# Kernel optimization log

Measured on AMD Instinct MI355X. Metric: run time of the kernel, lower is better.

Reference implementation:

```python
import jax, jax.numpy as jnp
import numpy as np


def setup_inputs() -> dict:
    key = jax.random.key(0)
    k1, k2 = jax.random.split(key)
    X_query = jax.random.normal(k1, (4, 4096, 32), dtype=jnp.float32)
    X_fit = jax.random.normal(k2, (4, 4096, 32), dtype=jnp.float32)
    return {"X_query": X_query, "X_fit": X_fit}


def _bandwidth(X_fit):
    # Silverman-style rule as in the torch module (bandwith init arg == 0.0)
    b, n, d = X_fit.shape
    flat = X_fit.reshape(b, -1)
    # torch.quantile with no dim reduces over the whole tensor -> scalar
    q = jnp.quantile(flat, 0.75) - jnp.quantile(flat, 0.25)
    std = jnp.std(X_fit, axis=(1, 2), ddof=1)  # torch.std is unbiased -> [b]
    return 0.9 * jnp.minimum(std, q / 1.34) / (n ** 0.2)  # [b]


def reference(X_query, X_fit):
    # fit()
    bw = _bandwidth(X_fit)                       # [b]
    nmu2 = jnp.sum(X_fit * X_fit, axis=-1)       # [b, m]
    # score()
    nx2 = jnp.sum(X_query * X_query, axis=-1, keepdims=True)   # [b, n, 1]
    dot = jnp.einsum('bnd,bmd->bnm', X_query, X_fit)           # [b, n, m]
    dist = nx2 + nmu2[:, None, :] - 2.0 * dot                  # [b, n, m]
    return jnp.sum(jnp.exp(-dist / bw[:, None, None]), axis=-1)  # [b, n]
```

## Files before the change

### kernel.cpp

```cpp
#include <hip/hip_runtime.h>
#include <hip/hip_bf16.h>
#include <math.h>

#define BB 4
#define MM 4096
#define DD 32
#define NSLOT 64

#define LOA -0.6945f
#define HIA -0.6545f
#define LOB  0.6545f
#define HIB  0.6945f

#define PSUM_OFF    0
#define PSUMSQ_OFF  1024
#define PBELA_OFF   2048
#define PBELB_OFF   3072
#define PCNTA_OFF   4096
#define PCNTB_OFF   5120
#define COEF_OFF    6144
#define CANDA_OFF   8192
#define CANDB_OFF   (CANDA_OFF + 65536)
#define NMU2_OFF    (CANDB_OFF + 65536)
#define NX2_OFF     (NMU2_OFF + 65536)
#define QH_OFF      (NX2_OFF + 65536)
#define QL_OFF      (QH_OFF + 1048576)
#define FH_OFF      (QL_OFF + 1048576)
#define FL_OFF      (FH_OFF + 1048576)

typedef short bf16x8 __attribute__((ext_vector_type(8)));
typedef float f32x4  __attribute__((ext_vector_type(4)));

__device__ __forceinline__ void cvt8(float4 a, float4 b, bf16x8* hi, bf16x8* lo) {
    union U { bf16x8 v; __hip_bfloat162 p[4]; };
    U H, L;
    float2 xs[4] = {make_float2(a.x,a.y), make_float2(a.z,a.w),
                    make_float2(b.x,b.y), make_float2(b.z,b.w)};
    #pragma unroll
    for (int i = 0; i < 4; i++) {
        __hip_bfloat162 h = __float22bfloat162_rn(xs[i]);
        float2 hf = __bfloat1622float2(h);
        H.p[i] = h;
        L.p[i] = __float22bfloat162_rn(make_float2(xs[i].x - hf.x, xs[i].y - hf.y));
    }
    *hi = H.v; *lo = L.v;
}

__global__ __launch_bounds__(256) void k_prep(
    const float* __restrict__ Xq, const float* __restrict__ Xf,
    short* __restrict__ Qh, short* __restrict__ Ql,
    short* __restrict__ Fh, short* __restrict__ Fl,
    float* __restrict__ nmu2, float* __restrict__ nx2,
    float* __restrict__ psum, float* __restrict__ psumsq,
    unsigned int* __restrict__ pbelA, unsigned int* __restrict__ pbelB,
    unsigned int* __restrict__ pcntA, unsigned int* __restrict__ pcntB,
    float* __restrict__ candA, float* __restrict__ candB)
{
    int tid = threadIdx.x;

    if (blockIdx.x >= 256) {
        int t = (blockIdx.x - 256) * 256 + tid;
        const float4* src = (const float4*)Xq + (size_t)t * 2;
        float4 v0 = src[0], v1 = src[1];
        bf16x8 hi, lo; cvt8(v0, v1, &hi, &lo);
        ((bf16x8*)Qh)[t] = hi;
        ((bf16x8*)Ql)[t] = lo;
        float xs[8] = {v0.x, v0.y, v0.z, v0.w, v1.x, v1.y, v1.z, v1.w};
        float s2 = 0.f;
        #pragma unroll
        for (int c = 0; c < 8; c++) s2 = fmaf(xs[c], xs[c], s2);
        s2 += __shfl_xor(s2, 1);
        s2 += __shfl_xor(s2, 2);
        if ((t & 3) == 0) nx2[t >> 2] = s2;
        return;
    }

    __shared__ float rs[256], rs2[256];
    __shared__ float lA[NSLOT], lB[NSLOT];
    __shared__ unsigned int lcA, lcB, lbA, lbB;
    if (tid == 0) { lcA = 0; lcB = 0; lbA = 0; lbB = 0; }
    __syncthreads();

    int blk = blockIdx.x;
    int t = blk * 256 + tid;
    const float4* src = (const float4*)Xf + (size_t)t * 2;
    float4 v0 = src[0], v1 = src[1];
    bf16x8 hi, lo; cvt8(v0, v1, &hi, &lo);
    ((bf16x8*)Fh)[t] = hi;
    ((bf16x8*)Fl)[t] = lo;

    float xs[8] = {v0.x, v0.y, v0.z, v0.w, v1.x, v1.y, v1.z, v1.w};
    float s = 0.f, s2 = 0.f;
    unsigned int belA = 0, belB = 0;
    #pragma unroll
    for (int c = 0; c < 8; c++) {
        float x = xs[c];
        s += x;
        s2 = fmaf(x, x, s2);
        belA += (x < LOA) ? 1u : 0u;
        belB += (x < LOB) ? 1u : 0u;
        if (x >= LOA && x < HIA) { unsigned int p = atomicAdd(&lcA, 1u); if (p < NSLOT) lA[p] = x; }
        if (x >= LOB && x < HIB) { unsigned int p = atomicAdd(&lcB, 1u); if (p < NSLOT) lB[p] = x; }
    }
    float r = s2;
    r += __shfl_xor(r, 1);
    r += __shfl_xor(r, 2);
    if ((t & 3) == 0) nmu2[t >> 2] = r;

    unsigned int wa = belA, wb = belB;
    #pragma unroll
    for (int m = 1; m < 64; m <<= 1) { wa += __shfl_xor(wa, m); wb += __shfl_xor(wb, m); }
    if ((tid & 63) == 0) { atomicAdd(&lbA, wa); atomicAdd(&lbB, wb); }

    rs[tid] = s; rs2[tid] = s2;
    __syncthreads();
    for (int off = 128; off > 0; off >>= 1) {
        if (tid < off) { rs[tid] += rs[tid + off]; rs2[tid] += rs2[tid + off]; }
        __syncthreads();
    }
    unsigned int na = lcA < (unsigned)NSLOT ? lcA : (unsigned)NSLOT;
    unsigned int nb = lcB < (unsigned)NSLOT ? lcB : (unsigned)NSLOT;
    if (tid == 0) {
        psum[blk]   = rs[0];
        psumsq[blk] = rs2[0];
        pbelA[blk]  = lbA;
        pbelB[blk]  = lbB;
        pcntA[blk]  = na;
        pcntB[blk]  = nb;
    }
    if (tid < (int)na) candA[blk * NSLOT + tid] = lA[tid];
    if (tid < (int)nb) candB[blk * NSLOT + tid] = lB[tid];
}

struct BwSh {
    unsigned int cnts[256];
    unsigned int hist[2048];
    unsigned int wsum[16];
    float gv[2][64];
    unsigned int gc[2];
    int binK[2];
    unsigned int baseK[2];
    float svals[4];
};

__global__ __launch_bounds__(1024) void k_bw(
    const float* __restrict__ psum, const float* __restrict__ psumsq,
    const unsigned int* __restrict__ pbelA, const unsigned int* __restrict__ pbelB,
    const unsigned int* __restrict__ pcntA, const unsigned int* __restrict__ pcntB,
    const float* __restrict__ candA, const float* __restrict__ candB,
    float* __restrict__ coef)
{
    __shared__ BwSh sh;
    int tid = threadIdx.x;
    int w = tid >> 6, lane = tid & 63;
    const float BSCALE = 2048.0f / (HIA - LOA);

    unsigned int ba = 0, bb = 0;
    if (tid < 256) { ba = pbelA[tid]; bb = pbelB[tid]; }
    #pragma unroll
    for (int m = 1; m < 64; m <<= 1) { ba += __shfl_xor(ba, m); bb += __shfl_xor(bb, m); }
    if (tid < 256 && lane == 0) { sh.wsum[w] = ba; sh.wsum[4 + w] = bb; }
    __syncthreads();
    unsigned int belowA = sh.wsum[0] + sh.wsum[1] + sh.wsum[2] + sh.wsum[3];
    unsigned int belowB = sh.wsum[4] + sh.wsum[5] + sh.wsum[6] + sh.wsum[7];
    __syncthreads();

    for (int s = 0; s < 2; s++) {
        const float* candS = s ? candB : candA;
        const unsigned int* pcnt = s ? pcntB : pcntA;
        float lo = s ? LOB : LOA;
        unsigned int below = s ? belowB : belowA;
        unsigned int k0 = (s ? 393215u : 131071u) - below;
        unsigned int k1 = k0 + 1;

        if (tid < 256) sh.cnts[tid] = pcnt[tid];
        for (int i = tid; i < 2048; i += 1024) sh.hist[i] = 0;
        if (tid == 0) { sh.gc[0] = 0; sh.gc[1] = 0; }
        __syncthreads();

        float vloc[16];
        bool  okloc[16];
        #pragma unroll
        for (int jj = 0; jj < 16; jj++) {
            int idx = jj * 1024 + tid;
            int blk = idx >> 6, slot = idx & 63;
            float v = candS[blk * NSLOT + slot];
            bool ok = (unsigned)slot < sh.cnts[blk];
            vloc[jj] = v; okloc[jj] = ok;
            if (ok) {
                int bn = (int)((v - lo) * BSCALE);
                bn = bn < 0 ? 0 : (bn > 2047 ? 2047 : bn);
                atomicAdd(&sh.hist[bn], 1u);
            }
        }
        __syncthreads();

        unsigned int b0 = sh.hist[2 * tid], b1 = sh.hist[2 * tid + 1];
        unsigned int own = b0 + b1;
        unsigned int inc = own;
        #pragma unroll
        for (int d = 1; d < 64; d <<= 1) {
            unsigned int t = __shfl_up(inc, d);
            if (lane >= d) inc += t;
        }
        if (lane == 63) sh.wsum[w] = inc;
        __syncthreads();
        if (tid < 16) {
            unsigned int x = sh.wsum[tid];
            #pragma unroll
            for (int d = 1; d < 16; d <<= 1) {
                unsigned int t = __shfl_up(x, d);
                if (tid >= d) x += t;
            }
            sh.wsum[tid] = x;
        }
        __syncthreads();
        unsigned int waveoff = (w == 0) ? 0u : sh.wsum[w - 1];
        unsigned int cum = waveoff + inc - own;
        if (cum <= k0 && k0 < cum + b0) { sh.binK[0] = 2 * tid;     sh.baseK[0] = cum; }
        if (cum <= k1 && k1 < cum + b0) { sh.binK[1] = 2 * tid;     sh.baseK[1] = cum; }
        cum += b0;
        if (cum <= k0 && k0 < cum + b1) { sh.binK[0] = 2 * tid + 1; sh.baseK[0] = cum; }
        if (cum <= k1 && k1 < cum + b1) { sh.binK[1] = 2 * tid + 1; sh.baseK[1] = cum; }
        __syncthreads();

        int bk0 = sh.binK[0], bk1 = sh.binK[1];
        #pragma unroll
        for (int jj = 0; jj < 16; jj++) {
            if (okloc[jj]) {
                float v = vloc[jj];
                int bn = (int)((v - lo) * BSCALE);
                bn = bn < 0 ? 0 : (bn > 2047 ? 2047 : bn);
                if (bn == bk0)               { unsigned int p = atomicAdd(&sh.gc[0], 1u); if (p < 64) sh.gv[0][p] = v; }
                if (bn == bk1 && bk1 != bk0) { unsigned int p = atomicAdd(&sh.gc[1], 1u); if (p < 64) sh.gv[1][p] = v; }
            }
        }
        __syncthreads();

        #pragma unroll
        for (int r = 0; r < 2; r++) {
            int src = (bk1 == bk0 && r == 1) ? 0 : r;
            unsigned int n = sh.gc[src]; if (n > 64u) n = 64u;
            unsigned int kk = (r ? k1 : k0) - sh.baseK[r];
            if ((unsigned int)tid < n) {
                float v = sh.gv[src][tid];
                unsigned int lt = 0, eq = 0;
                for (unsigned int j = 0; j < n; j++) {
                    float x = sh.gv[src][j];
                    lt += (x < v) ? 1u : 0u;
                    eq += (x == v) ? 1u : 0u;
                }
                if (lt <= kk && kk < lt + eq) sh.svals[s * 2 + r] = v;
            }
        }
        __syncthreads();
    }

    if (w < 4) {
        float ss = psum[w * 64 + lane], sq = psumsq[w * 64 + lane];
        #pragma unroll
        for (int m = 1; m < 64; m <<= 1) { ss += __shfl_xor(ss, m); sq += __shfl_xor(sq, m); }
        if (lane == 0) {
            float s0 = sh.svals[0], s1 = sh.svals[1];
            float s2v = sh.svals[2], s3 = sh.svals[3];
            double q25 = (double)s0 + 0.75 * ((double)s1 - (double)s0);
            double q75 = (double)s2v + 0.25 * ((double)s3 - (double)s2v);
            double q = q75 - q25;
            double n = (double)(MM * DD);
            double var = ((double)sq - (double)ss * (double)ss / n) / (n - 1.0);
            double sd = sqrt(var);
            double mn = sd < q / 1.34 ? sd : q / 1.34;
            double bwd = 0.9 * mn / 5.278031643091577;
            coef[w] = (float)(1.4426950408889634 / bwd);
        }
    }
}

__global__ __launch_bounds__(1024, 8) void k_kde(
    const short* __restrict__ Qh, const short* __restrict__ Ql,
    const short* __restrict__ Fh, const short* __restrict__ Fl,
    const float* __restrict__ nmu2, const float* __restrict__ nx2,
    const float* __restrict__ coef, float* __restrict__ out)
{
    __shared__ float red[16 * 32];
    int tid = threadIdx.x;
    int w = tid >> 6, lane = tid & 63;
    int b = blockIdx.x >> 7;
    int q0 = (blockIdx.x & 127) * 32;
    int m0 = w * 256;
    int l16 = lane & 15, quad = lane >> 4;

    const float c  = coef[b];
    const float c2 = 2.0f * c;

    const short* Qhb = Qh + ((size_t)b * MM + q0) * DD;
    const short* Qlb = Ql + ((size_t)b * MM + q0) * DD;
    bf16x8 Ah[2], Al[2];
    #pragma unroll
    for (int t = 0; t < 2; t++) {
        int off = (t * 16 + l16) * DD + quad * 8;
        Ah[t] = *(const bf16x8*)(Qhb + off);
        Al[t] = *(const bf16x8*)(Qlb + off);
    }
    const float* nxb = nx2 + b * MM + q0;
    float qz[2][4];
    #pragma unroll
    for (int t = 0; t < 2; t++)
        #pragma unroll
        for (int r = 0; r < 4; r++)
            qz[t][r] = -c * nxb[t * 16 + quad * 4 + r];

    float acc[2][4];
    #pragma unroll
    for (int t = 0; t < 2; t++)
        #pragma unroll
        for (int r = 0; r < 4; r++) acc[t][r] = 0.f;

    const short* Fhb = Fh + ((size_t)b * MM + m0) * DD;
    const short* Flb = Fl + ((size_t)b * MM + m0) * DD;
    const float* nmb = nmu2 + b * MM + m0;

    for (int mt = 0; mt < 16; ++mt) {
        int off = (mt * 16 + l16) * DD + quad * 8;
        bf16x8 Bh = *(const bf16x8*)(Fhb + off);
        bf16x8 Bl = *(const bf16x8*)(Flb + off);
        float wv = -c * nmb[mt * 16 + l16];
        #pragma unroll
        for (int t = 0; t < 2; t++) {
            f32x4 d = {0.f, 0.f, 0.f, 0.f};
            d = __builtin_amdgcn_mfma_f32_16x16x32_bf16(Al[t], Bh, d, 0, 0, 0);
            d = __builtin_amdgcn_mfma_f32_16x16x32_bf16(Ah[t], Bl, d, 0, 0, 0);
            d = __builtin_amdgcn_mfma_f32_16x16x32_bf16(Ah[t], Bh, d, 0, 0, 0);
            #pragma unroll
            for (int r = 0; r < 4; r++) {
                float arg = fmaf(c2, d[r], qz[t][r] + wv);
                acc[t][r] += __builtin_amdgcn_exp2f(arg);
            }
        }
    }

    #pragma unroll
    for (int t = 0; t < 2; t++)
        #pragma unroll
        for (int r = 0; r < 4; r++) {
            float v = acc[t][r];
            v += __shfl_xor(v, 1);
            v += __shfl_xor(v, 2);
            v += __shfl_xor(v, 4);
            v += __shfl_xor(v, 8);
            acc[t][r] = v;
        }

    int ts = (l16 >> 2) & 1, rs = l16 & 3;
    float val = 0.f;
    #pragma unroll
    for (int t = 0; t < 2; t++)
        #pragma unroll
        for (int r = 0; r < 4; r++)
            if (t == ts && r == rs) val = acc[t][r];
    if (l16 < 8) red[w * 32 + ts * 16 + quad * 4 + rs] = val;
    __syncthreads();
    if (tid < 32) {
        float s = 0.f;
        #pragma unroll
        for (int j = 0; j < 16; j++) s += red[j * 32 + tid];
        out[b * MM + q0 + tid] = s;
    }
}

extern "C" void kernel_launch(void* const* d_in, const int* in_sizes, int n_in,
                              void* d_out, int out_size, void* d_ws, size_t ws_size,
                              hipStream_t stream) {
    const float* Xq = (const float*)d_in[0];
    const float* Xf = (const float*)d_in[1];
    float* out = (float*)d_out;
    char* ws = (char*)d_ws;

    float* psum         = (float*)(ws + PSUM_OFF);
    float* psumsq       = (float*)(ws + PSUMSQ_OFF);
    unsigned int* pbelA = (unsigned int*)(ws + PBELA_OFF);
    unsigned int* pbelB = (unsigned int*)(ws + PBELB_OFF);
    unsigned int* pcntA = (unsigned int*)(ws + PCNTA_OFF);
    unsigned int* pcntB = (unsigned int*)(ws + PCNTB_OFF);
    float* coef         = (float*)(ws + COEF_OFF);
    float* candA        = (float*)(ws + CANDA_OFF);
    float* candB        = (float*)(ws + CANDB_OFF);
    float* nmu2         = (float*)(ws + NMU2_OFF);
    float* nx2          = (float*)(ws + NX2_OFF);
    short* Qh           = (short*)(ws + QH_OFF);
    short* Ql           = (short*)(ws + QL_OFF);
    short* Fh           = (short*)(ws + FH_OFF);
    short* Fl           = (short*)(ws + FL_OFF);

    k_prep<<<512, 256, 0, stream>>>(Xq, Xf, Qh, Ql, Fh, Fl, nmu2, nx2,
                                    psum, psumsq, pbelA, pbelB, pcntA, pcntB,
                                    candA, candB);
    k_bw<<<1, 1024, 0, stream>>>(psum, psumsq, pbelA, pbelB, pcntA, pcntB,
                                 candA, candB, coef);
    k_kde<<<512, 1024, 0, stream>>>(Qh, Ql, Fh, Fl, nmu2, nx2, coef, out);
}
```

Before: 102.5 us.

## Build global quantile histogram with atomics in prep, simplify bandwidth kernel

Quantile candidates are now binned straight into a global 2048-bin histogram with per-bin value slots, using global atomics during the prep kernel, in place of per-block candidate lists that the single-block bandwidth kernel re-histogrammed. The bandwidth kernel now only scans the bin counts and reads the selected bins' values, which shortens the serial one-block stage. The cost is a memset before launch and contention on global atomics. Values beyond 32 per bin are dropped, so a crowded bin could give a wrong quantile.

```diff
diff --git a/kernel.cpp b/kernel.cpp
--- a/kernel.cpp
+++ b/kernel.cpp
@@ -5,23 +5,22 @@
 #define BB 4
 #define MM 4096
 #define DD 32
-#define NSLOT 64
+#define SLOTS 32
 
 #define LOA -0.6945f
 #define HIA -0.6545f
 #define LOB  0.6545f
 #define HIB  0.6945f
+#define BSCALE 51200.0f
 
 #define PSUM_OFF    0
 #define PSUMSQ_OFF  1024
-#define PBELA_OFF   2048
-#define PBELB_OFF   3072
-#define PCNTA_OFF   4096
-#define PCNTB_OFF   5120
-#define COEF_OFF    6144
-#define CANDA_OFF   8192
-#define CANDB_OFF   (CANDA_OFF + 65536)
-#define NMU2_OFF    (CANDB_OFF + 65536)
+#define COEF_OFF    2048
+#define BEL_OFF     4096
+#define HCNT_OFF    4352
+#define ZERO_BYTES  (HCNT_OFF + 16384 - BEL_OFF)
+#define HVAL_OFF    32768
+#define NMU2_OFF    (HVAL_OFF + 524288)
 #define NX2_OFF     (NMU2_OFF + 65536)
 #define QH_OFF      (NX2_OFF + 65536)
 #define QL_OFF      (QH_OFF + 1048576)
@@ -52,9 +51,8 @@
     short* __restrict__ Fh, short* __restrict__ Fl,
     float* __restrict__ nmu2, float* __restrict__ nx2,
     float* __restrict__ psum, float* __restrict__ psumsq,
-    unsigned int* __restrict__ pbelA, unsigned int* __restrict__ pbelB,
-    unsigned int* __restrict__ pcntA, unsigned int* __restrict__ pcntB,
-    float* __restrict__ candA, float* __restrict__ candB)
+    unsigned int* __restrict__ bel, unsigned int* __restrict__ hcnt,
+    float* __restrict__ hval)
 {
     int tid = threadIdx.x;
 
@@ -76,11 +74,6 @@
     }
 
     __shared__ float rs[256], rs2[256];
-    __shared__ float lA[NSLOT], lB[NSLOT];
-    __shared__ unsigned int lcA, lcB, lbA, lbB;
-    if (tid == 0) { lcA = 0; lcB = 0; lbA = 0; lbB = 0; }
-    __syncthreads();
-
     int blk = blockIdx.x;
     int t = blk * 256 + tid;
     const float4* src = (const float4*)Xf + (size_t)t * 2;
@@ -99,8 +92,16 @@
         s2 = fmaf(x, x, s2);
         belA += (x < LOA) ? 1u : 0u;
         belB += (x < LOB) ? 1u : 0u;
-        if (x >= LOA && x < HIA) { unsigned int p = atomicAdd(&lcA, 1u); if (p < NSLOT) lA[p] = x; }
-        if (x >= LOB && x < HIB) { unsigned int p = atomicAdd(&lcB, 1u); if (p < NSLOT) lB[p] = x; }
+        if (x >= LOA && x < HIA) {
+            int bn = (int)((x - LOA) * BSCALE); if (bn > 2047) bn = 2047;
+            unsigned int p = atomicAdd(&hcnt[bn], 1u);
+            if (p < SLOTS) hval[bn * SLOTS + p] = x;
+        }
+        if (x >= LOB && x < HIB) {
+            int bn = (int)((x - LOB) * BSCALE); if (bn > 2047) bn = 2047;
+            unsigned int p = atomicAdd(&hcnt[2048 + bn], 1u);
+            if (p < SLOTS) hval[(2048 + bn) * SLOTS + p] = x;
+        }
     }
     float r = s2;
     r += __shfl_xor(r, 1);
@@ -110,7 +111,7 @@
     unsigned int wa = belA, wb = belB;
     #pragma unroll
     for (int m = 1; m < 64; m <<= 1) { wa += __shfl_xor(wa, m); wb += __shfl_xor(wb, m); }
-    if ((tid & 63) == 0) { atomicAdd(&lbA, wa); atomicAdd(&lbB, wb); }
+    if ((tid & 63) == 0) { atomicAdd(&bel[0], wa); atomicAdd(&bel[1], wb); }
 
     rs[tid] = s; rs2[tid] = s2;
     __syncthreads();
@@ -118,90 +119,44 @@
         if (tid < off) { rs[tid] += rs[tid + off]; rs2[tid] += rs2[tid + off]; }
         __syncthreads();
     }
-    unsigned int na = lcA < (unsigned)NSLOT ? lcA : (unsigned)NSLOT;
-    unsigned int nb = lcB < (unsigned)NSLOT ? lcB : (unsigned)NSLOT;
     if (tid == 0) {
         psum[blk]   = rs[0];
         psumsq[blk] = rs2[0];
-        pbelA[blk]  = lbA;
-        pbelB[blk]  = lbB;
-        pcntA[blk]  = na;
-        pcntB[blk]  = nb;
-    }
-    if (tid < (int)na) candA[blk * NSLOT + tid] = lA[tid];
-    if (tid < (int)nb) candB[blk * NSLOT + tid] = lB[tid];
+    }
 }
 
 struct BwSh {
-    unsigned int cnts[256];
-    unsigned int hist[2048];
     unsigned int wsum[16];
-    float gv[2][64];
-    unsigned int gc[2];
     int binK[2];
     unsigned int baseK[2];
+    unsigned int gn[2];
+    float gv[2][SLOTS];
     float svals[4];
 };
 
 __global__ __launch_bounds__(1024) void k_bw(
     const float* __restrict__ psum, const float* __restrict__ psumsq,
-    const unsigned int* __restrict__ pbelA, const unsigned int* __restrict__ pbelB,
-    const unsigned int* __restrict__ pcntA, const unsigned int* __restrict__ pcntB,
-    const float* __restrict__ candA, const float* __restrict__ candB,
+    const unsigned int* __restrict__ bel,
+    const unsigned int* __restrict__ hcnt, const float* __restrict__ hval,
     float* __restrict__ coef)
 {
     __shared__ BwSh sh;
     int tid = threadIdx.x;
     int w = tid >> 6, lane = tid & 63;
-    const float BSCALE = 2048.0f / (HIA - LOA);
-
-    unsigned int ba = 0, bb = 0;
-    if (tid < 256) { ba = pbelA[tid]; bb = pbelB[tid]; }
-    #pragma unroll
-    for (int m = 1; m < 64; m <<= 1) { ba += __shfl_xor(ba, m); bb += __shfl_xor(bb, m); }
-    if (tid < 256 && lane == 0) { sh.wsum[w] = ba; sh.wsum[4 + w] = bb; }
-    __syncthreads();
-    unsigned int belowA = sh.wsum[0] + sh.wsum[1] + sh.wsum[2] + sh.wsum[3];
-    unsigned int belowB = sh.wsum[4] + sh.wsum[5] + sh.wsum[6] + sh.wsum[7];
-    __syncthreads();
 
     for (int s = 0; s < 2; s++) {
-        const float* candS = s ? candB : candA;
-        const unsigned int* pcnt = s ? pcntB : pcntA;
-        float lo = s ? LOB : LOA;
-        unsigned int below = s ? belowB : belowA;
+        const unsigned int* cnt = hcnt + s * 2048;
+        unsigned int below = bel[s];
         unsigned int k0 = (s ? 393215u : 131071u) - below;
         unsigned int k1 = k0 + 1;
 
-        if (tid < 256) sh.cnts[tid] = pcnt[tid];
-        for (int i = tid; i < 2048; i += 1024) sh.hist[i] = 0;
-        if (tid == 0) { sh.gc[0] = 0; sh.gc[1] = 0; }
-        __syncthreads();
-
-        float vloc[16];
-        bool  okloc[16];
-        #pragma unroll
-        for (int jj = 0; jj < 16; jj++) {
-            int idx = jj * 1024 + tid;
-            int blk = idx >> 6, slot = idx & 63;
-            float v = candS[blk * NSLOT + slot];
-            bool ok = (unsigned)slot < sh.cnts[blk];
-            vloc[jj] = v; okloc[jj] = ok;
-            if (ok) {
-                int bn = (int)((v - lo) * BSCALE);
-                bn = bn < 0 ? 0 : (bn > 2047 ? 2047 : bn);
-                atomicAdd(&sh.hist[bn], 1u);
-            }
-        }
-        __syncthreads();
-
-        unsigned int b0 = sh.hist[2 * tid], b1 = sh.hist[2 * tid + 1];
+        unsigned int b0 = cnt[2 * tid], b1 = cnt[2 * tid + 1];
         unsigned int own = b0 + b1;
         unsigned int inc = own;
         #pragma unroll
         for (int d = 1; d < 64; d <<= 1) {
-            unsigned int t = __shfl_up(inc, d);
-            if (lane >= d) inc += t;
+            unsigned int tt = __shfl_up(inc, d);
+            if (lane >= d) inc += tt;
         }
         if (lane == 63) sh.wsum[w] = inc;
         __syncthreads();
@@ -209,8 +164,8 @@
             unsigned int x = sh.wsum[tid];
             #pragma unroll
             for (int d = 1; d < 16; d <<= 1) {
-                unsigned int t = __shfl_up(x, d);
-                if (tid >= d) x += t;
+                unsigned int tt = __shfl_up(x, d);
+                if (tid >= d) x += tt;
             }
             sh.wsum[tid] = x;
         }
@@ -224,29 +179,24 @@
         if (cum <= k1 && k1 < cum + b1) { sh.binK[1] = 2 * tid + 1; sh.baseK[1] = cum; }
         __syncthreads();
 
-        int bk0 = sh.binK[0], bk1 = sh.binK[1];
-        #pragma unroll
-        for (int jj = 0; jj < 16; jj++) {
-            if (okloc[jj]) {
-                float v = vloc[jj];
-                int bn = (int)((v - lo) * BSCALE);
-                bn = bn < 0 ? 0 : (bn > 2047 ? 2047 : bn);
-                if (bn == bk0)               { unsigned int p = atomicAdd(&sh.gc[0], 1u); if (p < 64) sh.gv[0][p] = v; }
-                if (bn == bk1 && bk1 != bk0) { unsigned int p = atomicAdd(&sh.gc[1], 1u); if (p < 64) sh.gv[1][p] = v; }
-            }
-        }
-        __syncthreads();
-
         #pragma unroll
         for (int r = 0; r < 2; r++) {
-            int src = (bk1 == bk0 && r == 1) ? 0 : r;
-            unsigned int n = sh.gc[src]; if (n > 64u) n = 64u;
+            int bin = sh.binK[r];
+            unsigned int n = cnt[bin]; if (n > (unsigned)SLOTS) n = SLOTS;
+            if ((unsigned int)tid < n) sh.gv[r][tid] = hval[(s * 2048 + bin) * SLOTS + tid];
+            if (tid == 0) sh.gn[r] = n;
+        }
+        __syncthreads();
+
+        #pragma unroll
+        for (int r = 0; r < 2; r++) {
+            unsigned int n = sh.gn[r];
             unsigned int kk = (r ? k1 : k0) - sh.baseK[r];
             if ((unsigned int)tid < n) {
-                float v = sh.gv[src][tid];
+                float v = sh.gv[r][tid];
                 unsigned int lt = 0, eq = 0;
                 for (unsigned int j = 0; j < n; j++) {
-                    float x = sh.gv[src][j];
+                    float x = sh.gv[r][j];
                     lt += (x < v) ? 1u : 0u;
                     eq += (x == v) ? 1u : 0u;
                 }
@@ -378,13 +328,10 @@
 
     float* psum         = (float*)(ws + PSUM_OFF);
     float* psumsq       = (float*)(ws + PSUMSQ_OFF);
-    unsigned int* pbelA = (unsigned int*)(ws + PBELA_OFF);
-    unsigned int* pbelB = (unsigned int*)(ws + PBELB_OFF);
-    unsigned int* pcntA = (unsigned int*)(ws + PCNTA_OFF);
-    unsigned int* pcntB = (unsigned int*)(ws + PCNTB_OFF);
     float* coef         = (float*)(ws + COEF_OFF);
-    float* candA        = (float*)(ws + CANDA_OFF);
-    float* candB        = (float*)(ws + CANDB_OFF);
+    unsigned int* bel   = (unsigned int*)(ws + BEL_OFF);
+    unsigned int* hcnt  = (unsigned int*)(ws + HCNT_OFF);
+    float* hval         = (float*)(ws + HVAL_OFF);
     float* nmu2         = (float*)(ws + NMU2_OFF);
     float* nx2          = (float*)(ws + NX2_OFF);
     short* Qh           = (short*)(ws + QH_OFF);
@@ -392,10 +339,10 @@
     short* Fh           = (short*)(ws + FH_OFF);
     short* Fl           = (short*)(ws + FL_OFF);
 
+    hipMemsetAsync(ws + BEL_OFF, 0, ZERO_BYTES, stream);
+
     k_prep<<<512, 256, 0, stream>>>(Xq, Xf, Qh, Ql, Fh, Fl, nmu2, nx2,
-                                    psum, psumsq, pbelA, pbelB, pcntA, pcntB,
-                                    candA, candB);
-    k_bw<<<1, 1024, 0, stream>>>(psum, psumsq, pbelA, pbelB, pcntA, pcntB,
-                                 candA, candB, coef);
+                                    psum, psumsq, bel, hcnt, hval);
+    k_bw<<<1, 1024, 0, stream>>>(psum, psumsq, bel, hcnt, hval, coef);
     k_kde<<<512, 1024, 0, stream>>>(Qh, Ql, Fh, Fl, nmu2, nx2, coef, out);
 }
```

After: 115.0 us. +12.1%, slower.
